# Kernel tuning notes

Measured on AMD Instinct MI355X. Metric: run time of the kernel, lower is better.

The kernel has to match this reference:

```python
import jax, jax.numpy as jnp
import numpy as np
import math

N = 40000
E = 1280000
HID = 128
NF = 128
NG = 50
L = 3
CUTOFF = 10.0


def ssp(x):
    # shifted softplus: softplus(x) - log(2)
    return jax.nn.softplus(x) - jnp.float32(math.log(2.0))


def setup_inputs() -> dict:
    key = jax.random.key(0)
    ks = jax.random.split(key, 16)
    z = jax.random.randint(ks[0], (N,), 0, 100)
    pos = jax.random.normal(ks[1], (N, 3), dtype=jnp.float32) * 3.0
    batch = jnp.zeros((N,), dtype=jnp.int32)
    edge_index = jax.random.randint(ks[2], (2, E), 0, N)
    s = 0.1
    emb = jax.random.normal(ks[3], (100, HID), dtype=jnp.float32) * s
    mlp_w1 = jax.random.normal(ks[4], (L, NG, NF), dtype=jnp.float32) * s
    mlp_b1 = jnp.zeros((L, NF), dtype=jnp.float32)
    mlp_w2 = jax.random.normal(ks[5], (L, NF, NF), dtype=jnp.float32) * s
    mlp_b2 = jnp.zeros((L, NF), dtype=jnp.float32)
    conv_w1 = jax.random.normal(ks[6], (L, HID, NF), dtype=jnp.float32) * s  # no bias
    conv_w2 = jax.random.normal(ks[7], (L, NF, HID), dtype=jnp.float32) * s
    conv_b2 = jnp.zeros((L, HID), dtype=jnp.float32)
    lin_w = jax.random.normal(ks[8], (L, HID, HID), dtype=jnp.float32) * s
    lin_b = jnp.zeros((L, HID), dtype=jnp.float32)
    lin1_w = jax.random.normal(ks[9], (HID, HID // 2), dtype=jnp.float32) * s
    lin1_b = jnp.zeros((HID // 2,), dtype=jnp.float32)
    return {
        "z": z, "pos": pos, "batch": batch, "edge_index": edge_index,
        "emb": emb, "mlp_w1": mlp_w1, "mlp_b1": mlp_b1, "mlp_w2": mlp_w2,
        "mlp_b2": mlp_b2, "conv_w1": conv_w1, "conv_w2": conv_w2,
        "conv_b2": conv_b2, "lin_w": lin_w, "lin_b": lin_b,
        "lin1_w": lin1_w, "lin1_b": lin1_b,
    }


def reference(z, pos, batch, edge_index, emb, mlp_w1, mlp_b1, mlp_w2, mlp_b2,
              conv_w1, conv_w2, conv_b2, lin_w, lin_b, lin1_w, lin1_b):
    n = z.shape[0]
    row, col = edge_index[0], edge_index[1]
    # edge distances (radius-graph edge weights)
    diff = pos[row] - pos[col]                       # [E,3]
    edge_weight = jnp.sqrt(jnp.sum(diff * diff, axis=-1))  # [E]
    # Gaussian smearing
    offset = jnp.linspace(0.0, CUTOFF, NG, dtype=jnp.float32)
    coeff = -0.5 / (offset[1] - offset[0]) ** 2
    edge_attr = jnp.exp(coeff * (edge_weight[:, None] - offset[None, :]) ** 2)  # [E,NG]
    # cosine cutoff
    C = 0.5 * (jnp.cos(edge_weight * (jnp.pi / CUTOFF)) + 1.0)  # [E]

    h = emb[z]  # [N,HID]
    for l in range(L):
        W = ssp(edge_attr @ mlp_w1[l] + mlp_b1[l]) @ mlp_w2[l] + mlp_b2[l]  # [E,NF]
        W = W * C[:, None]
        x = h @ conv_w1[l]                      # [N,NF]
        msg = x[row] * W                        # gather + filter, [E,NF]
        agg = jax.ops.segment_sum(msg, col, num_segments=n)  # scatter-add, [N,NF]
        x = agg @ conv_w2[l] + conv_b2[l]       # [N,HID]
        x = ssp(x)
        x = x @ lin_w[l] + lin_b[l]
        h = h + x
    return ssp(h @ lin1_w + lin1_b)  # [N,HID//2]
```

## Files before the change

### kernel.cpp

```cpp
#include <hip/hip_runtime.h>
#include <math.h>


typedef _Float16 f16;
typedef _Float16 half8 __attribute__((ext_vector_type(8)));
typedef _Float16 half4v __attribute__((ext_vector_type(4)));
typedef float f32x4 __attribute__((ext_vector_type(4)));

#define NGAUSS 50
#define HIDF   128
#define NBINS  8192
#define DMAXF  40.0f
#define NLAYER 3
#define XST    132
#define BSHIFT 7
#define NPB    128
#define MAXBUCK 512
#define SCAP  5120

static __device__ __forceinline__ float sspf(float v) {
    return fmaxf(v, 0.0f) + log1pf(expf(-fabsf(v))) - 0.6931471805599453f;
}

__global__ __launch_bounds__(256) void k_stage(const int* __restrict__ ei,
                                               const float* __restrict__ pos,
                                               int* __restrict__ scnt,
                                               uint2* __restrict__ staging,
                                               int E, int nbuck) {
    const float SCALE = (float)(NBINS - 1) / DMAXF;
    __shared__ int bhist[MAXBUCK];
    __shared__ int boff[MAXBUCK];
    __shared__ int gpos[MAXBUCK];
    __shared__ uint2 recs[4096];
    __shared__ unsigned short lbuck[4096];
    int t = threadIdx.x;
    for (int i = t; i < MAXBUCK; i += 256) bhist[i] = 0;
    __syncthreads();
    int e0 = blockIdx.x * 4096;
    int cnt_here = min(4096, E - e0);
    unsigned pay[16];
    unsigned short cc[16];
    short rk[16];
#pragma unroll
    for (int k = 0; k < 16; ++k) {
        int idx = t + k * 256;
        rk[k] = -1;
        if (idx < cnt_here) {
            int e = e0 + idx;
            int r = ei[e], c = ei[E + e];
            float dx = pos[3*r+0] - pos[3*c+0];
            float dy = pos[3*r+1] - pos[3*c+1];
            float dz = pos[3*r+2] - pos[3*c+2];
            float d = sqrtf(dx*dx + dy*dy + dz*dz);
            float u = fminf(d * SCALE, (float)(NBINS - 1));
            int i0 = min((int)u, NBINS - 2);
            float w0 = u - (float)i0;
            int wq = (int)(w0 * 8.0f + 0.5f);
            if (wq == 8) { i0 = min(i0 + 1, NBINS - 2); wq = 0; }
            pay[k] = ((unsigned)i0 << 19) | ((unsigned)wq << 16) | (unsigned)r;
            cc[k] = (unsigned short)c;
            rk[k] = (short)atomicAdd(&bhist[c >> BSHIFT], 1);
        }
    }
    __syncthreads();
    if (t < 64) {
        int base = t * 8;
        int s[8];
        int run = 0;
#pragma unroll
        for (int j = 0; j < 8; ++j) { s[j] = run; run += bhist[base + j]; }
        int incl = run;
        for (int o = 1; o < 64; o <<= 1) {
            int v = __shfl_up(incl, o, 64);
            if (t >= o) incl += v;
        }
        int excl = incl - run;
#pragma unroll
        for (int j = 0; j < 8; ++j) boff[base + j] = excl + s[j];
    }
    __syncthreads();
    for (int i = t; i < nbuck; i += 256) gpos[i] = atomicAdd(&scnt[i], bhist[i]);
#pragma unroll
    for (int k = 0; k < 16; ++k) {
        if (rk[k] >= 0) {
            int b = cc[k] >> BSHIFT;
            int slot = boff[b] + rk[k];
            recs[slot] = make_uint2(pay[k], (unsigned)cc[k]);
            lbuck[slot] = (unsigned short)b;
        }
    }
    __syncthreads();
    for (int i = t; i < cnt_here; i += 256) {
        int b = lbuck[i];
        staging[(size_t)b * SCAP + gpos[b] + (i - boff[b])] = recs[i];
    }
}

__global__ __launch_bounds__(1024) void k_place(const uint2* __restrict__ staging,
                                                const int* __restrict__ scnt,
                                                int* __restrict__ meta,
                                                int* __restrict__ offs,
                                                int n, int nbuck) {
    __shared__ int lcnt[NPB], loff[NPB], lcur[NPB];
    __shared__ int ldsm[SCAP];
    __shared__ int wsum[16];
    __shared__ int ebase_s;
    int b = blockIdx.x, t = threadIdx.x;
    int cntb = scnt[b];
    int part = 0;
    for (int j = t; j < b; j += 1024) part += scnt[j];
    for (int o = 32; o > 0; o >>= 1) part += __shfl_down(part, o, 64);
    if ((t & 63) == 0) wsum[t >> 6] = part;
    if (t < NPB) { lcnt[t] = 0; lcur[t] = 0; }
    __syncthreads();
    if (t == 0) {
        int r = 0;
        for (int w = 0; w < 16; ++w) r += wsum[w];
        ebase_s = r;
    }
    const uint2* sb = staging + (size_t)b * SCAP;
    for (int i = t; i < cntb; i += 1024)
        atomicAdd(&lcnt[sb[i].y & (NPB - 1)], 1);
    __syncthreads();
    int ebase = ebase_s;
    if (t < NPB) loff[t] = lcnt[t];
    __syncthreads();
    for (int o = 1; o < NPB; o <<= 1) {
        int v = 0;
        if (t < NPB) { v = loff[t]; if (t >= o) v += loff[t - o]; }
        __syncthreads();
        if (t < NPB) loff[t] = v;
        __syncthreads();
    }
    int nb0 = b << BSHIFT;
    if (t < NPB) {
        int node = nb0 + t;
        if (node < n) offs[node] = ebase + loff[t] - lcnt[t];
    }
    if (b == nbuck - 1 && t == 0) offs[n] = ebase + cntb;
    __syncthreads();
    for (int i = t; i < cntb; i += 1024) {
        uint2 r = sb[i];
        int cl = (int)(r.y & (NPB - 1));
        int lpos = (loff[cl] - lcnt[cl]) + atomicAdd(&lcur[cl], 1);
        if (lpos < SCAP) ldsm[lpos] = (int)r.x;
        else meta[ebase + lpos] = (int)r.x;
    }
    __syncthreads();
    int lim = min(cntb, SCAP);
    for (int i = t; i < lim; i += 1024) meta[ebase + i] = ldsm[i];
}

__global__ __launch_bounds__(128) void k_table(const float* __restrict__ w1,
                                               const float* __restrict__ b1,
                                               const float* __restrict__ w2,
                                               const float* __restrict__ b2,
                                               f16* __restrict__ T) {
    const float DELTA = 10.0f / 49.0f;
    const float COEFF = -0.5f / (DELTA * DELTA);
    const float HSTEP = DMAXF / (float)(NBINS - 1);
    __shared__ float ea[8][NGAUSS];
    __shared__ float u[8][HIDF];
    int l = blockIdx.y, b0 = blockIdx.x * 8, j = threadIdx.x;
    for (int idx = j; idx < 8 * NGAUSS; idx += 128) {
        int bb = idx / NGAUSS, g = idx % NGAUSS;
        float d = (float)(b0 + bb) * HSTEP;
        float diff = d - (float)g * DELTA;
        ea[bb][g] = expf(COEFF * diff * diff);
    }
    __syncthreads();
    float acc[8];
    {
        float bias = b1[l * HIDF + j];
#pragma unroll
        for (int b = 0; b < 8; ++b) acc[b] = bias;
        const float* w1l = w1 + (size_t)l * NGAUSS * HIDF;
        for (int g = 0; g < NGAUSS; ++g) {
            float wv = w1l[g * HIDF + j];
#pragma unroll
            for (int b = 0; b < 8; ++b) acc[b] = fmaf(ea[b][g], wv, acc[b]);
        }
#pragma unroll
        for (int b = 0; b < 8; ++b) u[b][j] = sspf(acc[b]);
    }
    __syncthreads();
    {
        float bias = b2[l * HIDF + j];
#pragma unroll
        for (int b = 0; b < 8; ++b) acc[b] = bias;
        const float* w2l = w2 + (size_t)l * HIDF * HIDF;
        for (int k = 0; k < HIDF; ++k) {
            float wv = w2l[k * HIDF + j];
#pragma unroll
            for (int b = 0; b < 8; ++b) acc[b] = fmaf(u[b][k], wv, acc[b]);
        }
    }
    f16* Tl = T + ((size_t)l * NBINS + b0) * HIDF;
#pragma unroll
    for (int b = 0; b < 8; ++b) {
        float d = (float)(b0 + b) * HSTEP;
        float C = 0.5f * (cosf(d * (float)(M_PI / 10.0)) + 1.0f);
        Tl[b * HIDF + j] = (f16)(acc[b] * C);
    }
}

__global__ void k_wpack(const float* __restrict__ cw1, const float* __restrict__ cw2,
                        const float* __restrict__ lw, const float* __restrict__ l1w,
                        f16* __restrict__ Wp) {
    int mat = blockIdx.y;
    int N = (mat == 9) ? 64 : HIDF;
    int ntiles = N >> 4;
    int tid = blockIdx.x * 256 + threadIdx.x;
    int lane = tid & 63, ks = (tid >> 6) & 3, nt = tid >> 8;
    if (nt >= ntiles) return;
    const float* W;
    if (mat < 9) {
        int l = mat / 3, kind = mat % 3;
        W = (kind == 0 ? cw1 : kind == 1 ? cw2 : lw) + (size_t)l * HIDF * HIDF;
    } else {
        W = l1w;
    }
    int kbase = ks * 32 + (lane >> 4) * 8;
    int col = nt * 16 + (lane & 15);
    half8 st;
#pragma unroll
    for (int j = 0; j < 8; ++j) st[j] = (f16)W[(size_t)(kbase + j) * N + col];
    *(half8*)&Wp[(size_t)mat * 16384 + ((size_t)(nt * 4 + ks) * 64 + lane) * 8] = st;
}

#define AGG_EDGE(yy)                                                         \
    {                                                                        \
        int row_ = (yy) & 0xFFFF;                                            \
        int i0_ = ((unsigned)(yy)) >> 19;                                    \
        float w0_ = (float)(((yy) >> 16) & 7) * 0.125f;                      \
        half8 x0_ = *(const half8*)&xj[(size_t)row_ * HIDF];                 \
        half8 ta_ = *(const half8*)&Tj[(size_t)i0_ * HIDF];                  \
        half8 tb_ = *(const half8*)&Tj[(size_t)(i0_ + 1) * HIDF];            \
        _Pragma("unroll")                                                    \
        for (int j = 0; j < 8; ++j) {                                        \
            float t0 = (float)ta_[j];                                        \
            float f0 = fmaf(w0_, (float)tb_[j] - t0, t0);                    \
            a[j] = fmaf((float)x0_[j], f0, a[j]);                            \
        }                                                                    \
    }

__global__ __launch_bounds__(256) void k_agg(const f16* __restrict__ x,
                                             const f16* __restrict__ T,
                                             const int* __restrict__ meta,
                                             const int* __restrict__ offs,
                                             f16* __restrict__ agg, int n) {
    int node = (blockIdx.x * blockDim.x + threadIdx.x) >> 4;
    int lane = threadIdx.x & 15;
    if (node >= n) return;
    int beg = offs[node], end = offs[node + 1];
    const f16* xj = x + lane * 8;
    const f16* Tj = T + lane * 8;
    float a[8] = {};
    for (int chunk = beg; chunk < end; chunk += 16) {
        int cnt = min(16, end - chunk);
        int mm = meta[chunk + min(lane, cnt - 1)];
        int q = 0;
        for (; q + 4 <= cnt; q += 4) {
            int y0 = __shfl(mm, q + 0, 16);
            int y1 = __shfl(mm, q + 1, 16);
            int y2 = __shfl(mm, q + 2, 16);
            int y3 = __shfl(mm, q + 3, 16);
            AGG_EDGE(y0)
            AGG_EDGE(y1)
            AGG_EDGE(y2)
            AGG_EDGE(y3)
        }
        for (; q < cnt; ++q) {
            int y0 = __shfl(mm, q, 16);
            AGG_EDGE(y0)
        }
    }
    half8 st;
#pragma unroll
    for (int j = 0; j < 8; ++j) st[j] = (f16)a[j];
    *(half8*)&agg[(size_t)node * HIDF + lane * 8] = st;
}

__global__ __launch_bounds__(256) void k_init_gemm(const int* __restrict__ z,
                                                   const float* __restrict__ emb,
                                                   const f16* __restrict__ w1p,
                                                   f16* __restrict__ xout) {
    int lane = threadIdx.x & 63;
    int wid = threadIdx.x >> 6;
    int m0 = blockIdx.x * 64 + wid * 16;
    int mrow = lane & 15, quad = lane >> 4;
    const float* er = emb + (size_t)z[m0 + mrow] * HIDF + quad * 8;
    half8 afr[4];
#pragma unroll
    for (int ks = 0; ks < 4; ++ks) {
        float4 a = *(const float4*)(er + ks * 32);
        float4 b = *(const float4*)(er + ks * 32 + 4);
        half8 f = {(f16)a.x, (f16)a.y, (f16)a.z, (f16)a.w,
                   (f16)b.x, (f16)b.y, (f16)b.z, (f16)b.w};
        afr[ks] = f;
    }
    f32x4 acc[8];
#pragma unroll
    for (int t = 0; t < 8; ++t) acc[t] = (f32x4){0.f, 0.f, 0.f, 0.f};
    const f16* bp = w1p + (size_t)lane * 8;
#pragma unroll
    for (int t = 0; t < 8; ++t)
#pragma unroll
        for (int ks = 0; ks < 4; ++ks) {
            half8 bfr = *(const half8*)(bp + (size_t)(t * 4 + ks) * 512);
            acc[t] = __builtin_amdgcn_mfma_f32_16x16x32_f16(afr[ks], bfr, acc[t], 0, 0, 0);
        }
    int col0 = lane & 15;
    int growb = m0 + quad * 4;
#pragma unroll
    for (int t = 0; t < 8; ++t)
#pragma unroll
        for (int r = 0; r < 4; ++r)
            xout[(size_t)(growb + r) * HIDF + t * 16 + col0] = (f16)acc[t][r];
}

template <int NT3, bool LAYER0, bool WRITE_H>
__global__ __launch_bounds__(256) void k_fused(const f16* __restrict__ agg,
                                               const f16* __restrict__ w2p,
                                               const float* __restrict__ b2,
                                               const f16* __restrict__ lwp,
                                               const float* __restrict__ lb,
                                               const f16* __restrict__ b3p,
                                               const float* __restrict__ b3,
                                               float* __restrict__ hio,
                                               const int* __restrict__ z,
                                               const float* __restrict__ emb,
                                               f16* __restrict__ xout,
                                               float* __restrict__ fout) {
    __shared__ f16 Xs[4][16][XST];
    int lane = threadIdx.x & 63;
    int wid = threadIdx.x >> 6;
    int m0 = blockIdx.x * 64 + wid * 16;
    int mrow = lane & 15, quad = lane >> 4;
    int col0 = mrow;
    int growb = m0 + quad * 4;
    f16 (*X)[XST] = Xs[wid];

    half8 afr[4];
    {
        const f16* Ar = agg + (size_t)(m0 + mrow) * HIDF + quad * 8;
#pragma unroll
        for (int ks = 0; ks < 4; ++ks) afr[ks] = *(const half8*)(Ar + ks * 32);
    }
    f32x4 acc[8];
#pragma unroll
    for (int t = 0; t < 8; ++t) acc[t] = (f32x4){0.f, 0.f, 0.f, 0.f};
    {
        const f16* bp = w2p + (size_t)lane * 8;
#pragma unroll
        for (int t = 0; t < 8; ++t)
#pragma unroll
            for (int ks = 0; ks < 4; ++ks) {
                half8 bfr = *(const half8*)(bp + (size_t)(t * 4 + ks) * 512);
                acc[t] = __builtin_amdgcn_mfma_f32_16x16x32_f16(afr[ks], bfr, acc[t], 0, 0, 0);
            }
    }
#pragma unroll
    for (int t = 0; t < 8; ++t) {
        int col = t * 16 + col0;
        float bv = b2[col];
#pragma unroll
        for (int r = 0; r < 4; ++r)
            X[quad * 4 + r][col] = (f16)sspf(acc[t][r] + bv);
    }
#pragma unroll
    for (int ks = 0; ks < 4; ++ks) {
        half4v lo = *(const half4v*)&X[mrow][ks * 32 + quad * 8];
        half4v hi = *(const half4v*)&X[mrow][ks * 32 + quad * 8 + 4];
        half8 f;
#pragma unroll
        for (int j = 0; j < 4; ++j) { f[j] = lo[j]; f[4 + j] = hi[j]; }
        afr[ks] = f;
    }
#pragma unroll
    for (int t = 0; t < 8; ++t) acc[t] = (f32x4){0.f, 0.f, 0.f, 0.f};
    {
        const f16* bp = lwp + (size_t)lane * 8;
#pragma unroll
        for (int t = 0; t < 8; ++t)
#pragma unroll
            for (int ks = 0; ks < 4; ++ks) {
                half8 bfr = *(const half8*)(bp + (size_t)(t * 4 + ks) * 512);
                acc[t] = __builtin_amdgcn_mfma_f32_16x16x32_f16(afr[ks], bfr, acc[t], 0, 0, 0);
            }
    }
    int zr[4];
    if (LAYER0) {
#pragma unroll
        for (int r = 0; r < 4; ++r) zr[r] = z[growb + r];
    }
#pragma unroll
    for (int t = 0; t < 8; ++t) {
        int col = t * 16 + col0;
        float bv = lb[col];
#pragma unroll
        for (int r = 0; r < 4; ++r) {
            int grow = growb + r;
            float resid = LAYER0 ? emb[(size_t)zr[r] * HIDF + col]
                                 : hio[(size_t)grow * HIDF + col];
            float hp = acc[t][r] + bv + resid;
            if (WRITE_H) hio[(size_t)grow * HIDF + col] = hp;
            X[quad * 4 + r][col] = (f16)hp;
        }
    }
#pragma unroll
    for (int ks = 0; ks < 4; ++ks) {
        half4v lo = *(const half4v*)&X[mrow][ks * 32 + quad * 8];
        half4v hi = *(const half4v*)&X[mrow][ks * 32 + quad * 8 + 4];
        half8 f;
#pragma unroll
        for (int j = 0; j < 4; ++j) { f[j] = lo[j]; f[4 + j] = hi[j]; }
        afr[ks] = f;
    }
#pragma unroll
    for (int t = 0; t < NT3; ++t) acc[t] = (f32x4){0.f, 0.f, 0.f, 0.f};
    {
        const f16* bp = b3p + (size_t)lane * 8;
#pragma unroll
        for (int t = 0; t < NT3; ++t)
#pragma unroll
            for (int ks = 0; ks < 4; ++ks) {
                half8 bfr = *(const half8*)(bp + (size_t)(t * 4 + ks) * 512);
                acc[t] = __builtin_amdgcn_mfma_f32_16x16x32_f16(afr[ks], bfr, acc[t], 0, 0, 0);
            }
    }
    if (NT3 == 8) {
#pragma unroll
        for (int t = 0; t < 8; ++t)
#pragma unroll
            for (int r = 0; r < 4; ++r)
                xout[(size_t)(growb + r) * HIDF + t * 16 + col0] = (f16)acc[t][r];
    } else {
#pragma unroll
        for (int t = 0; t < NT3; ++t) {
            int col = t * 16 + col0;
            float bv = b3[col];
#pragma unroll
            for (int r = 0; r < 4; ++r)
                fout[(size_t)(growb + r) * (NT3 * 16) + col] = sspf(acc[t][r] + bv);
        }
    }
}

extern "C" void kernel_launch(void* const* d_in, const int* in_sizes, int n_in,
                              void* d_out, int out_size, void* d_ws, size_t ws_size,
                              hipStream_t stream) {
    const int*   z       = (const int*)d_in[0];
    const float* pos     = (const float*)d_in[1];
    const int*   ei      = (const int*)d_in[3];
    const float* emb     = (const float*)d_in[4];
    const float* mlp_w1  = (const float*)d_in[5];
    const float* mlp_b1  = (const float*)d_in[6];
    const float* mlp_w2  = (const float*)d_in[7];
    const float* mlp_b2  = (const float*)d_in[8];
    const float* conv_w1 = (const float*)d_in[9];
    const float* conv_w2 = (const float*)d_in[10];
    const float* conv_b2 = (const float*)d_in[11];
    const float* lin_w   = (const float*)d_in[12];
    const float* lin_b   = (const float*)d_in[13];
    const float* lin1_w  = (const float*)d_in[14];
    const float* lin1_b  = (const float*)d_in[15];
    float* out = (float*)d_out;

    int n = in_sizes[0];
    int E = in_sizes[3] / 2;
    int nbuck = (n + NPB - 1) >> BSHIFT;

    char* ws = (char*)d_ws;
    size_t off = 0;
    auto alloc = [&](size_t bytes) -> void* {
        void* p = ws + off;
        off = (off + bytes + 255) & ~(size_t)255;
        return p;
    };
    float* h     = (float*)alloc((size_t)n * HIDF * 4);
    f16*   x16   = (f16*)alloc((size_t)n * HIDF * 2);
    f16*   agg16 = (f16*)alloc((size_t)n * HIDF * 2);
    f16*   T16   = (f16*)alloc((size_t)NLAYER * NBINS * HIDF * 2);
    int*   meta  = (int*)alloc((size_t)E * 4);
    int*   offs  = (int*)alloc((size_t)(n + 1) * 4);
    int*   scnt  = (int*)alloc((size_t)nbuck * 4);
    uint2* staging = (uint2*)alloc((size_t)nbuck * SCAP * 8);
    f16*   Wp    = (f16*)alloc((size_t)10 * 16384 * 2);

    const int tb = 256;
    hipMemsetAsync(scnt, 0, (size_t)nbuck * 4, stream);
    hipLaunchKernelGGL(k_stage, dim3((E + 4095) / 4096), dim3(tb), 0, stream,
                       ei, pos, scnt, staging, E, nbuck);
    hipLaunchKernelGGL(k_place, dim3(nbuck), dim3(1024), 0, stream,
                       staging, scnt, meta, offs, n, nbuck);
    hipLaunchKernelGGL(k_wpack, dim3(8, 10), dim3(tb), 0, stream,
                       conv_w1, conv_w2, lin_w, lin1_w, Wp);
    hipLaunchKernelGGL(k_table, dim3(NBINS / 8, NLAYER), dim3(128), 0, stream,
                       mlp_w1, mlp_b1, mlp_w2, mlp_b2, T16);

    int gemmblocks = n / 64;
    int aggblocks = (n * 16 + tb - 1) / tb;
    hipLaunchKernelGGL(k_init_gemm, dim3(gemmblocks), dim3(tb), 0, stream,
                       z, emb, Wp + (size_t)0 * 16384, x16);
    hipLaunchKernelGGL(k_agg, dim3(aggblocks), dim3(tb), 0, stream,
                       x16, T16 + (size_t)0 * NBINS * HIDF, meta, offs, agg16, n);
    hipLaunchKernelGGL(HIP_KERNEL_NAME(k_fused<8, true, true>), dim3(gemmblocks), dim3(tb), 0, stream,
                       agg16, Wp + (size_t)1 * 16384, conv_b2 + 0 * HIDF,
                       Wp + (size_t)2 * 16384, lin_b + 0 * HIDF,
                       Wp + (size_t)3 * 16384, (const float*)nullptr,
                       h, z, emb, x16, (float*)nullptr);
    hipLaunchKernelGGL(k_agg, dim3(aggblocks), dim3(tb), 0, stream,
                       x16, T16 + (size_t)1 * NBINS * HIDF, meta, offs, agg16, n);
    hipLaunchKernelGGL(HIP_KERNEL_NAME(k_fused<8, false, true>), dim3(gemmblocks), dim3(tb), 0, stream,
                       agg16, Wp + (size_t)4 * 16384, conv_b2 + 1 * HIDF,
                       Wp + (size_t)5 * 16384, lin_b + 1 * HIDF,
                       Wp + (size_t)6 * 16384, (const float*)nullptr,
                       h, (const int*)nullptr, (const float*)nullptr, x16, (float*)nullptr);
    hipLaunchKernelGGL(k_agg, dim3(aggblocks), dim3(tb), 0, stream,
                       x16, T16 + (size_t)2 * NBINS * HIDF, meta, offs, agg16, n);
    hipLaunchKernelGGL(HIP_KERNEL_NAME(k_fused<4, false, false>), dim3(gemmblocks), dim3(tb), 0, stream,
                       agg16, Wp + (size_t)7 * 16384, conv_b2 + 2 * HIDF,
                       Wp + (size_t)8 * 16384, lin_b + 2 * HIDF,
                       Wp + (size_t)9 * 16384, lin1_b,
                       h, (const int*)nullptr, (const float*)nullptr, (f16*)nullptr, out);
    (void)n_in; (void)out_size; (void)ws_size;
}
```

Before: 514.4 us.

## Split fused GEMM chain output columns across wave pairs to double block count

Each 16-row tile in the fused three-GEMM kernel is now handled by two waves, each computing half of the output columns, with 32 rows per block instead of 64. Intermediate activations are shared through LDS with block barriers between stages. The goal is more blocks and fewer accumulators per wave, giving better occupancy on the 40k-row problem. The cost is extra __syncthreads, duplicated A-fragment loads, and more total blocks.

```diff
diff --git a/kernel.cpp b/kernel.cpp
--- a/kernel.cpp
+++ b/kernel.cpp
@@ -332,14 +332,16 @@
                                                const float* __restrict__ emb,
                                                f16* __restrict__ xout,
                                                float* __restrict__ fout) {
-    __shared__ f16 Xs[4][16][XST];
+    __shared__ f16 Xs[2][16][XST];
     int lane = threadIdx.x & 63;
     int wid = threadIdx.x >> 6;
-    int m0 = blockIdx.x * 64 + wid * 16;
+    int rt = wid >> 1;
+    int ch = wid & 1;
+    int m0 = blockIdx.x * 32 + rt * 16;
     int mrow = lane & 15, quad = lane >> 4;
     int col0 = mrow;
     int growb = m0 + quad * 4;
-    f16 (*X)[XST] = Xs[wid];
+    f16 (*X)[XST] = Xs[rt];
 
     half8 afr[4];
     {
@@ -347,27 +349,28 @@
 #pragma unroll
         for (int ks = 0; ks < 4; ++ks) afr[ks] = *(const half8*)(Ar + ks * 32);
     }
-    f32x4 acc[8];
-#pragma unroll
-    for (int t = 0; t < 8; ++t) acc[t] = (f32x4){0.f, 0.f, 0.f, 0.f};
+    f32x4 acc[4];
+#pragma unroll
+    for (int t = 0; t < 4; ++t) acc[t] = (f32x4){0.f, 0.f, 0.f, 0.f};
     {
         const f16* bp = w2p + (size_t)lane * 8;
 #pragma unroll
-        for (int t = 0; t < 8; ++t)
+        for (int t = 0; t < 4; ++t)
 #pragma unroll
             for (int ks = 0; ks < 4; ++ks) {
-                half8 bfr = *(const half8*)(bp + (size_t)(t * 4 + ks) * 512);
+                half8 bfr = *(const half8*)(bp + (size_t)((ch * 4 + t) * 4 + ks) * 512);
                 acc[t] = __builtin_amdgcn_mfma_f32_16x16x32_f16(afr[ks], bfr, acc[t], 0, 0, 0);
             }
     }
 #pragma unroll
-    for (int t = 0; t < 8; ++t) {
-        int col = t * 16 + col0;
+    for (int t = 0; t < 4; ++t) {
+        int col = ch * 64 + t * 16 + col0;
         float bv = b2[col];
 #pragma unroll
         for (int r = 0; r < 4; ++r)
             X[quad * 4 + r][col] = (f16)sspf(acc[t][r] + bv);
     }
+    __syncthreads();
 #pragma unroll
     for (int ks = 0; ks < 4; ++ks) {
         half4v lo = *(const half4v*)&X[mrow][ks * 32 + quad * 8];
@@ -377,15 +380,16 @@
         for (int j = 0; j < 4; ++j) { f[j] = lo[j]; f[4 + j] = hi[j]; }
         afr[ks] = f;
     }
-#pragma unroll
-    for (int t = 0; t < 8; ++t) acc[t] = (f32x4){0.f, 0.f, 0.f, 0.f};
+    __syncthreads();
+#pragma unroll
+    for (int t = 0; t < 4; ++t) acc[t] = (f32x4){0.f, 0.f, 0.f, 0.f};
     {
         const f16* bp = lwp + (size_t)lane * 8;
 #pragma unroll
-        for (int t = 0; t < 8; ++t)
+        for (int t = 0; t < 4; ++t)
 #pragma unroll
             for (int ks = 0; ks < 4; ++ks) {
-                half8 bfr = *(const half8*)(bp + (size_t)(t * 4 + ks) * 512);
+                half8 bfr = *(const half8*)(bp + (size_t)((ch * 4 + t) * 4 + ks) * 512);
                 acc[t] = __builtin_amdgcn_mfma_f32_16x16x32_f16(afr[ks], bfr, acc[t], 0, 0, 0);
             }
     }
@@ -395,8 +399,8 @@
         for (int r = 0; r < 4; ++r) zr[r] = z[growb + r];
     }
 #pragma unroll
-    for (int t = 0; t < 8; ++t) {
-        int col = t * 16 + col0;
+    for (int t = 0; t < 4; ++t) {
+        int col = ch * 64 + t * 16 + col0;
         float bv = lb[col];
 #pragma unroll
         for (int r = 0; r < 4; ++r) {
@@ -408,6 +412,7 @@
             X[quad * 4 + r][col] = (f16)hp;
         }
     }
+    __syncthreads();
 #pragma unroll
     for (int ks = 0; ks < 4; ++ks) {
         half4v lo = *(const half4v*)&X[mrow][ks * 32 + quad * 8];
@@ -417,28 +422,29 @@
         for (int j = 0; j < 4; ++j) { f[j] = lo[j]; f[4 + j] = hi[j]; }
         afr[ks] = f;
     }
-#pragma unroll
-    for (int t = 0; t < NT3; ++t) acc[t] = (f32x4){0.f, 0.f, 0.f, 0.f};
+    constexpr int TH = NT3 / 2;
+#pragma unroll
+    for (int t = 0; t < TH; ++t) acc[t] = (f32x4){0.f, 0.f, 0.f, 0.f};
     {
         const f16* bp = b3p + (size_t)lane * 8;
 #pragma unroll
-        for (int t = 0; t < NT3; ++t)
+        for (int t = 0; t < TH; ++t)
 #pragma unroll
             for (int ks = 0; ks < 4; ++ks) {
-                half8 bfr = *(const half8*)(bp + (size_t)(t * 4 + ks) * 512);
+                half8 bfr = *(const half8*)(bp + (size_t)((ch * TH + t) * 4 + ks) * 512);
                 acc[t] = __builtin_amdgcn_mfma_f32_16x16x32_f16(afr[ks], bfr, acc[t], 0, 0, 0);
             }
     }
     if (NT3 == 8) {
 #pragma unroll
-        for (int t = 0; t < 8; ++t)
+        for (int t = 0; t < TH; ++t)
 #pragma unroll
             for (int r = 0; r < 4; ++r)
-                xout[(size_t)(growb + r) * HIDF + t * 16 + col0] = (f16)acc[t][r];
+                xout[(size_t)(growb + r) * HIDF + ch * 64 + t * 16 + col0] = (f16)acc[t][r];
     } else {
 #pragma unroll
-        for (int t = 0; t < NT3; ++t) {
-            int col = t * 16 + col0;
+        for (int t = 0; t < TH; ++t) {
+            int col = ch * 32 + t * 16 + col0;
             float bv = b3[col];
 #pragma unroll
             for (int r = 0; r < 4; ++r)
@@ -500,26 +506,27 @@
                        mlp_w1, mlp_b1, mlp_w2, mlp_b2, T16);
 
     int gemmblocks = n / 64;
+    int fusedblocks = n / 32;
     int aggblocks = (n * 16 + tb - 1) / tb;
     hipLaunchKernelGGL(k_init_gemm, dim3(gemmblocks), dim3(tb), 0, stream,
                        z, emb, Wp + (size_t)0 * 16384, x16);
     hipLaunchKernelGGL(k_agg, dim3(aggblocks), dim3(tb), 0, stream,
                        x16, T16 + (size_t)0 * NBINS * HIDF, meta, offs, agg16, n);
-    hipLaunchKernelGGL(HIP_KERNEL_NAME(k_fused<8, true, true>), dim3(gemmblocks), dim3(tb), 0, stream,
+    hipLaunchKernelGGL(HIP_KERNEL_NAME(k_fused<8, true, true>), dim3(fusedblocks), dim3(tb), 0, stream,
                        agg16, Wp + (size_t)1 * 16384, conv_b2 + 0 * HIDF,
                        Wp + (size_t)2 * 16384, lin_b + 0 * HIDF,
                        Wp + (size_t)3 * 16384, (const float*)nullptr,
                        h, z, emb, x16, (float*)nullptr);
     hipLaunchKernelGGL(k_agg, dim3(aggblocks), dim3(tb), 0, stream,
                        x16, T16 + (size_t)1 * NBINS * HIDF, meta, offs, agg16, n);
-    hipLaunchKernelGGL(HIP_KERNEL_NAME(k_fused<8, false, true>), dim3(gemmblocks), dim3(tb), 0, stream,
+    hipLaunchKernelGGL(HIP_KERNEL_NAME(k_fused<8, false, true>), dim3(fusedblocks), dim3(tb), 0, stream,
                        agg16, Wp + (size_t)4 * 16384, conv_b2 + 1 * HIDF,
                        Wp + (size_t)5 * 16384, lin_b + 1 * HIDF,
                        Wp + (size_t)6 * 16384, (const float*)nullptr,
                        h, (const int*)nullptr, (const float*)nullptr, x16, (float*)nullptr);
     hipLaunchKernelGGL(k_agg, dim3(aggblocks), dim3(tb), 0, stream,
                        x16, T16 + (size_t)2 * NBINS * HIDF, meta, offs, agg16, n);
-    hipLaunchKernelGGL(HIP_KERNEL_NAME(k_fused<4, false, false>), dim3(gemmblocks), dim3(tb), 0, stream,
+    hipLaunchKernelGGL(HIP_KERNEL_NAME(k_fused<4, false, false>), dim3(fusedblocks), dim3(tb), 0, stream,
                        agg16, Wp + (size_t)7 * 16384, conv_b2 + 2 * HIDF,
                        Wp + (size_t)8 * 16384, lin_b + 2 * HIDF,
                        Wp + (size_t)9 * 16384, lin1_b,
```

Measured after the change: 416.6 us. 19.0% less time.
